# Optimization experiments

Hardware: AMD Instinct MI355X
Metric: run time of the kernel (lower is better)

## Reference

```python
import jax, jax.numpy as jnp
import numpy as np

NUM_HEADS = 4

def setup_inputs() -> dict:
    key = jax.random.key(0)
    ks = jax.random.split(key, 8)
    B_, N, C = 4096, 49, 128
    nW = 64
    return {
        "x": jax.random.normal(ks[0], (B_, N, C), dtype=jnp.float32),
        "mask": jax.random.normal(ks[1], (nW, N, N), dtype=jnp.float32),
        "qkv_w": jax.random.normal(ks[2], (3 * C, C), dtype=jnp.float32) * 0.02,
        "qkv_b": jax.random.normal(ks[3], (3 * C,), dtype=jnp.float32) * 0.02,
        "proj_w": jax.random.normal(ks[4], (C, C), dtype=jnp.float32) * 0.02,
        "proj_b": jax.random.normal(ks[5], (C,), dtype=jnp.float32) * 0.02,
        "rpb_table": jax.random.normal(ks[6], (169, NUM_HEADS), dtype=jnp.float32) * 0.02,
        "rel_index": jax.random.randint(ks[7], (N, N), 0, 169, dtype=jnp.int64),
    }

def reference(x, mask, qkv_w, qkv_b, proj_w, proj_b, rpb_table, rel_index):
    B_, N, C = x.shape
    H = NUM_HEADS
    hd = C // H
    scale = hd ** -0.5
    # qkv projection: [B_, N, 3, H, hd] -> (3, B_, H, N, hd)
    qkv = (x @ qkv_w.T + qkv_b).reshape(B_, N, 3, H, hd).transpose(2, 0, 3, 1, 4)
    q, k, v = qkv[0], qkv[1], qkv[2]
    q = q * scale
    attn = jnp.einsum('bhnd,bhmd->bhnm', q, k)  # [B_, H, N, N]
    # relative position bias gather: [N*N, H] -> [H, N, N]
    bias = rpb_table[rel_index.reshape(-1)].reshape(N, N, H).transpose(2, 0, 1)
    attn = attn + bias[None]
    # window mask add: view (B_//nW, nW, H, N, N) + mask[None, :, None]
    nW = mask.shape[0]
    attn = attn.reshape(B_ // nW, nW, H, N, N) + mask[None, :, None]
    attn = attn.reshape(B_, H, N, N)
    attn = jax.nn.softmax(attn, axis=-1)
    out = jnp.einsum('bhnm,bhmd->bhnd', attn, v)  # [B_, H, N, hd]
    out = out.transpose(0, 2, 1, 3).reshape(B_, N, C)
    out = out @ proj_w.T + proj_b
    return out
```

## Files before the change

### kernel.cpp

```cpp
#include <hip/hip_runtime.h>
#include <stdint.h>

typedef __attribute__((ext_vector_type(4))) float f32x4;
typedef __attribute__((ext_vector_type(2))) float f32x2;
typedef __attribute__((ext_vector_type(8))) short s16x8;
typedef __attribute__((ext_vector_type(4))) short s16x4;
typedef __attribute__((ext_vector_type(8))) __bf16 bf16x8;
typedef __attribute__((ext_vector_type(2))) __bf16 bf16x2;
typedef __attribute__((ext_vector_type(2))) unsigned u32x2;

#define SCALE 0.17677669529663687f
#define LOG2E 1.4426950408889634f

__device__ __forceinline__ unsigned f2bf(float f) {
  unsigned u = __builtin_bit_cast(unsigned, f);
  u += 0x7fffu + ((u >> 16) & 1u);
  return u >> 16;
}
__device__ __forceinline__ unsigned pk2(float lo, float hi) {
  f32x2 v; v[0] = lo; v[1] = hi;
  bf16x2 h = __builtin_convertvector(v, bf16x2);
  return __builtin_bit_cast(unsigned, h);
}
__device__ __forceinline__ unsigned short cv1(float v) {
  return (unsigned short)f2bf(v);
}

__device__ __forceinline__ f32x4 MFMA(s16x8 a, s16x8 b, f32x4 c) {
  return __builtin_amdgcn_mfma_f32_16x16x32_bf16(
      __builtin_bit_cast(bf16x8, a), __builtin_bit_cast(bf16x8, b), c, 0, 0, 0);
}
__device__ __forceinline__ f32x4 MFMA16(u32x2 a, u32x2 b, f32x4 c) {
#if __has_builtin(__builtin_amdgcn_mfma_f32_16x16x16bf16_1k)
  return __builtin_amdgcn_mfma_f32_16x16x16bf16_1k(
      __builtin_bit_cast(s16x4, a), __builtin_bit_cast(s16x4, b), c, 0, 0, 0);
#else
  f32x4 d;
  asm("v_mfma_f32_16x16x16_bf16 %0, %1, %2, %3"
      : "=v"(d) : "v"(a), "v"(b), "v"(c));
  return d;
#endif
}

template <int MODE>
__global__ __launch_bounds__(256, 4)
void win_attn(const float* __restrict__ x,
              const float* __restrict__ mask,
              const float* __restrict__ qkv_bs,
              const float* __restrict__ proj_b,
              const unsigned short* __restrict__ wq_bf,
              const unsigned short* __restrict__ wp_bf,
              const float* __restrict__ bias_full,
              const float* __restrict__ bias_pad,
              const float* __restrict__ mask_pad,
              const float* __restrict__ comb,
              float* __restrict__ out) {
  __shared__ alignas(16) char smem[16384];
  const int tid = threadIdx.x;
  const int l = tid & 63, w = tid >> 6;
  const int lr = l & 15, lq = l >> 4;
  const int b = blockIdx.x;
  const int wq = b & 63;

  {
    const float* xw = x + (size_t)b * (49 * 128);
    #pragma unroll
    for (int i = 0; i < 4; ++i) {
      const int r = w * 4 + lq + i * 16;
      s16x8 v = {};
      if (r < 49) {
        const float4* p = reinterpret_cast<const float4*>(xw + r * 128 + lr * 8);
        float4 f0 = p[0], f1 = p[1];
        union { unsigned u[4]; s16x8 v8; } U;
        U.u[0] = pk2(f0.x, f0.y); U.u[1] = pk2(f0.z, f0.w);
        U.u[2] = pk2(f1.x, f1.y); U.u[3] = pk2(f1.z, f1.w);
        v = U.v8;
      }
      *reinterpret_cast<s16x8*>(&smem[r * 256 + (((lr ^ (r & 15)) & 15) << 4)]) = v;
    }
  }
  __syncthreads();

  int addrK[4];
  #pragma unroll
  for (int kt = 0; kt < 4; ++kt)
    addrK[kt] = lr * 256 + ((((4 * kt + lq) ^ lr) & 15) << 4);

  u32x2 qB[4][2], kB[4][2], vA[2][4];
  #pragma unroll
  for (int g = 0; g < 6; ++g) {
    const int sect = g >> 1;
    const int half = g & 1;
    const int obase = sect * 128 + 32 * w + 16 * half;
    s16x8 wf[4];
    #pragma unroll
    for (int kt = 0; kt < 4; ++kt)
      wf[kt] = *reinterpret_cast<const s16x8*>(wq_bf + (obase + lr) * 128 + kt * 32 + lq * 8);
    if (sect < 2) {
      const f32x4 bia4 = *reinterpret_cast<const f32x4*>(qkv_bs + obase + 4 * lq);
      #pragma unroll
      for (int nt = 0; nt < 4; ++nt) {
        s16x8 ar[4];
        #pragma unroll
        for (int kt = 0; kt < 4; ++kt)
          ar[kt] = *reinterpret_cast<const s16x8*>(&smem[addrK[kt] + nt * 4096]);
        f32x4 acc = {};
        #pragma unroll
        for (int kt = 0; kt < 4; ++kt) acc = MFMA(wf[kt], ar[kt], acc);
        acc += bia4;
        u32x2 fr; fr[0] = pk2(acc[0], acc[1]); fr[1] = pk2(acc[2], acc[3]);
        if (sect == 0) qB[nt][half] = fr; else kB[nt][half] = fr;
      }
    } else {
      const float bo = qkv_bs[obase + lr];
      #pragma unroll
      for (int mt = 0; mt < 4; ++mt) {
        s16x8 ar[4];
        #pragma unroll
        for (int kt = 0; kt < 4; ++kt)
          ar[kt] = *reinterpret_cast<const s16x8*>(&smem[addrK[kt] + mt * 4096]);
        f32x4 acc = {};
        #pragma unroll
        for (int kt = 0; kt < 4; ++kt) acc = MFMA(ar[kt], wf[kt], acc);
        acc += bo;
        u32x2 fr; fr[0] = pk2(acc[0], acc[1]); fr[1] = pk2(acc[2], acc[3]);
        vA[half][mt] = fr;
      }
    }
  }
  __syncthreads();

  const float* biaW = bias_pad + w * 4096;
  const float* mskW = mask_pad + wq * 4096;
  const float* cW = comb + (size_t)(wq * 4 + w) * 4096;
  #pragma unroll
  for (int ntn = 0; ntn < 4; ++ntn) {
    const int n = 16 * ntn + lr;
    f32x4 add4[4];
    if (MODE == 2) {
      #pragma unroll
      for (int mtm = 0; mtm < 4; ++mtm)
        add4[mtm] = *reinterpret_cast<const f32x4*>(cW + n * 64 + 16 * mtm + 4 * lq);
    } else if (MODE == 1) {
      #pragma unroll
      for (int mtm = 0; mtm < 4; ++mtm) {
        const int m0 = 16 * mtm + 4 * lq;
        f32x4 bb = *reinterpret_cast<const f32x4*>(biaW + n * 64 + m0);
        f32x4 mm = *reinterpret_cast<const f32x4*>(mskW + n * 64 + m0);
        add4[mtm] = bb + mm;
      }
    }
    f32x4 sacc[4];
    __builtin_amdgcn_s_setprio(1);
    #pragma unroll
    for (int mtm = 0; mtm < 4; ++mtm) {
      sacc[mtm] = MFMA16(kB[mtm][0], qB[ntn][0], f32x4{});
      sacc[mtm] = MFMA16(kB[mtm][1], qB[ntn][1], sacc[mtm]);
    }
    __builtin_amdgcn_s_setprio(0);
    if (MODE >= 1) {
      #pragma unroll
      for (int mtm = 0; mtm < 4; ++mtm) sacc[mtm] += add4[mtm];
    } else {
      #pragma unroll
      for (int mtm = 0; mtm < 4; ++mtm)
        #pragma unroll
        for (int j = 0; j < 4; ++j) {
          const int m = 16 * mtm + 4 * lq + j;
          if (m < 49 && n < 49)
            sacc[mtm][j] = fmaf(bias_full[w * 2401 + n * 49 + m] + mask[wq * 2401 + n * 49 + m],
                                LOG2E, sacc[mtm][j]);
        }
    }
    {
      f32x4 v = sacc[3];
      v[0] = (lq == 0) ? v[0] : -1e30f;
      v[1] = -1e30f; v[2] = -1e30f; v[3] = -1e30f;
      sacc[3] = v;
    }
    float mx = -1e30f;
    #pragma unroll
    for (int mtm = 0; mtm < 4; ++mtm) {
      f32x4 v = sacc[mtm];
      mx = fmaxf(mx, fmaxf(fmaxf(v[0], v[1]), fmaxf(v[2], v[3])));
    }
    mx = fmaxf(mx, __shfl_xor(mx, 16, 64));
    mx = fmaxf(mx, __shfl_xor(mx, 32, 64));
    float s = 0.f;
    #pragma unroll
    for (int mtm = 0; mtm < 4; ++mtm) {
      f32x4 v = sacc[mtm];
      #pragma unroll
      for (int j = 0; j < 4; ++j) { v[j] = __builtin_exp2f(v[j] - mx); s += v[j]; }
      sacc[mtm] = v;
    }
    s += __shfl_xor(s, 16, 64);
    s += __shfl_xor(s, 32, 64);
    const float ri = 1.f / s;
    u32x2 p[4];
    #pragma unroll
    for (int mtm = 0; mtm < 4; ++mtm) {
      p[mtm][0] = pk2(sacc[mtm][0], sacc[mtm][1]);
      p[mtm][1] = pk2(sacc[mtm][2], sacc[mtm][3]);
    }
    __builtin_amdgcn_s_setprio(1);
    #pragma unroll
    for (int dt = 0; dt < 2; ++dt) {
      f32x4 oc = {};
      #pragma unroll
      for (int mtm = 0; mtm < 4; ++mtm) oc = MFMA16(vA[dt][mtm], p[mtm], oc);
      oc *= ri;
      u32x2 ov; ov[0] = pk2(oc[0], oc[1]); ov[1] = pk2(oc[2], oc[3]);
      const int cb = 64 * w + 32 * dt + 8 * lq;
      *reinterpret_cast<u32x2*>(
          &smem[n * 256 + (((((cb >> 4) ^ lr) & 15) << 4) | (cb & 15))]) = ov;
    }
    __builtin_amdgcn_s_setprio(0);
  }
  __syncthreads();

  s16x8 wpf[2][4];
  #pragma unroll
  for (int ct = 0; ct < 2; ++ct)
    #pragma unroll
    for (int kt = 0; kt < 4; ++kt)
      wpf[ct][kt] = *reinterpret_cast<const s16x8*>(
          wp_bf + (32 * w + 16 * ct + lr) * 128 + kt * 32 + lq * 8);
  float* ob = out + (size_t)b * (49 * 128);
  #pragma unroll
  for (int nt = 0; nt < 4; ++nt) {
    const int n = 16 * nt + lr;
    s16x8 osf[4];
    #pragma unroll
    for (int kt = 0; kt < 4; ++kt) {
      const int cb = 64 * kt + 16 * lq;
      osf[kt] = *reinterpret_cast<const s16x8*>(
          &smem[n * 256 + (((((cb >> 4) ^ lr) & 15) << 4) | (cb & 15))]);
    }
    #pragma unroll
    for (int ct = 0; ct < 2; ++ct) {
      const int c0 = 32 * w + 16 * ct + 4 * lq;
      f32x4 acc = {};
      #pragma unroll
      for (int kt = 0; kt < 4; ++kt) acc = MFMA(wpf[ct][kt], osf[kt], acc);
      acc += *reinterpret_cast<const f32x4*>(proj_b + c0);
      if (n < 49) *reinterpret_cast<f32x4*>(ob + n * 128 + c0) = acc;
    }
  }
}

__global__ void prep_kernel(const float* __restrict__ qkv_w,
                            const float* __restrict__ qkv_b,
                            const float* __restrict__ proj_w,
                            const float* __restrict__ rpb,
                            const int* __restrict__ rel_raw,
                            const float* __restrict__ mask,
                            unsigned short* __restrict__ wq_bf,
                            unsigned short* __restrict__ wp_bf,
                            float* __restrict__ qkv_bs,
                            float* __restrict__ bias_full,
                            float* __restrict__ bias_pad,
                            float* __restrict__ mask_pad,
                            float* __restrict__ comb,
                            int mode) {
  const int i = blockIdx.x * 256 + threadIdx.x;
  if (i < 49152) {
    float v = qkv_w[i];
    if (i < 16384) v *= SCALE * LOG2E;
    wq_bf[i] = cv1(v);
  } else if (i < 65536) {
    wp_bf[i - 49152] = cv1(proj_w[i - 49152]);
  } else if (i < 65920) {
    const int t = i - 65536;
    float v = qkv_b[t];
    if (t < 128) v *= SCALE * LOG2E;
    qkv_bs[t] = v;
  } else if (i < 75524) {
    const int t = i - 65920;
    const int h = t / 2401, nm = t % 2401;
    const bool is64 = (rel_raw[1] == 0) && (rel_raw[3] == 0) &&
                      (rel_raw[5] == 0) && (rel_raw[7] == 0);
    const int ridx = is64 ? rel_raw[2 * nm] : rel_raw[nm];
    bias_full[t] = rpb[ridx * 4 + h];
  } else if (mode == 2 && i < 75524 + 1048576) {
    const int t = i - 75524;
    const int wqi = t >> 14, h = (t >> 12) & 3, n = (t >> 6) & 63, m = t & 63;
    float v = 0.f;
    if (n < 49 && m < 49) {
      const bool is64 = (rel_raw[1] == 0) && (rel_raw[3] == 0) &&
                        (rel_raw[5] == 0) && (rel_raw[7] == 0);
      const int nm = n * 49 + m;
      const int ridx = is64 ? rel_raw[2 * nm] : rel_raw[nm];
      v = (rpb[ridx * 4 + h] + mask[wqi * 2401 + nm]) * LOG2E;
    }
    comb[t] = v;
  } else if (mode == 1 && i < 75524 + 16384) {
    const int j = i - 75524;
    const int h = j >> 12, r = (j >> 6) & 63, m = j & 63;
    float v = 0.f;
    if (r < 49 && m < 49) {
      const bool is64 = (rel_raw[1] == 0) && (rel_raw[3] == 0) &&
                        (rel_raw[5] == 0) && (rel_raw[7] == 0);
      const int nm = r * 49 + m;
      const int ridx = is64 ? rel_raw[2 * nm] : rel_raw[nm];
      v = rpb[ridx * 4 + h] * LOG2E;
    }
    bias_pad[j] = v;
  } else if (mode == 1 && i < 75524 + 16384 + 262144) {
    const int t = i - 75524 - 16384;
    const int wqi = t >> 12, n = (t >> 6) & 63, m = t & 63;
    mask_pad[t] = (n < 49 && m < 49) ? mask[wqi * 2401 + n * 49 + m] * LOG2E : 0.f;
  }
}

extern "C" void kernel_launch(void* const* d_in, const int* in_sizes, int n_in,
                              void* d_out, int out_size, void* d_ws, size_t ws_size,
                              hipStream_t stream) {
  const float* x      = (const float*)d_in[0];
  const float* mask   = (const float*)d_in[1];
  const float* qkv_w  = (const float*)d_in[2];
  const float* qkv_b  = (const float*)d_in[3];
  const float* proj_w = (const float*)d_in[4];
  const float* proj_b = (const float*)d_in[5];
  const float* rpb    = (const float*)d_in[6];
  const int*   rel    = (const int*)d_in[7];
  float* out = (float*)d_out;

  char* ws = (char*)d_ws;
  unsigned short* wq_bf = (unsigned short*)(ws + 0);
  unsigned short* wp_bf = (unsigned short*)(ws + 98304);
  float* qkv_bs    = (float*)(ws + 131072);
  float* bias_full = (float*)(ws + 132608);
  float* bias_pad  = (float*)(ws + 171024);
  float* mask_pad  = (float*)(ws + 236560);
  float* comb      = (float*)(ws + 1285376);

  int mode = 0;
  if (ws_size >= 5479680) mode = 2;
  else if (ws_size >= 1285136) mode = 1;
  const int B_ = in_sizes[0] / (49 * 128);

  const int prep_n = 75524 + (mode == 2 ? 1048576 : mode == 1 ? (16384 + 262144) : 0);
  prep_kernel<<<(prep_n + 255) / 256, 256, 0, stream>>>(
      qkv_w, qkv_b, proj_w, rpb, rel, mask,
      wq_bf, wp_bf, qkv_bs, bias_full, bias_pad, mask_pad, comb, mode);
  if (mode == 2)
    win_attn<2><<<B_, 256, 0, stream>>>(x, mask, qkv_bs, proj_b, wq_bf, wp_bf,
                                        bias_full, bias_pad, mask_pad, comb, out);
  else if (mode == 1)
    win_attn<1><<<B_, 256, 0, stream>>>(x, mask, qkv_bs, proj_b, wq_bf, wp_bf,
                                        bias_full, bias_pad, mask_pad, comb, out);
  else
    win_attn<0><<<B_, 256, 0, stream>>>(x, mask, qkv_bs, proj_b, wq_bf, wp_bf,
                                        bias_full, bias_pad, mask_pad, comb, out);
}
```

Measured before the change: 125.6 us.

## Cut register pressure to raise occupancy: split bias loads, drop softmax max, reload proj weights

Raises the launch-bounds occupancy hint from 4 to 5 blocks per CU. To fit in fewer registers, it loads the bias/mask additive terms in two halves interleaved with the QK MFMAs, and loads projection weight fragments per output tile instead of holding all of them. It also removes the row-max subtraction from the softmax and exponentiates the raw scores directly, which saves a reduction and two shuffles. Skipping the max relies on logits staying bounded, so larger inputs could overflow exp2.

```diff
diff --git a/kernel.cpp b/kernel.cpp
--- a/kernel.cpp
+++ b/kernel.cpp
@@ -43,7 +43,7 @@
 }
 
 template <int MODE>
-__global__ __launch_bounds__(256, 4)
+__global__ __launch_bounds__(256, 5)
 void win_attn(const float* __restrict__ x,
               const float* __restrict__ mask,
               const float* __restrict__ qkv_bs,
@@ -136,31 +136,44 @@
   #pragma unroll
   for (int ntn = 0; ntn < 4; ++ntn) {
     const int n = 16 * ntn + lr;
-    f32x4 add4[4];
+    f32x4 sacc[4];
+    f32x4 add2[2];
     if (MODE == 2) {
-      #pragma unroll
-      for (int mtm = 0; mtm < 4; ++mtm)
-        add4[mtm] = *reinterpret_cast<const f32x4*>(cW + n * 64 + 16 * mtm + 4 * lq);
+      add2[0] = *reinterpret_cast<const f32x4*>(cW + n * 64 + 4 * lq);
+      add2[1] = *reinterpret_cast<const f32x4*>(cW + n * 64 + 16 + 4 * lq);
     } else if (MODE == 1) {
-      #pragma unroll
-      for (int mtm = 0; mtm < 4; ++mtm) {
-        const int m0 = 16 * mtm + 4 * lq;
-        f32x4 bb = *reinterpret_cast<const f32x4*>(biaW + n * 64 + m0);
-        f32x4 mm = *reinterpret_cast<const f32x4*>(mskW + n * 64 + m0);
-        add4[mtm] = bb + mm;
-      }
-    }
-    f32x4 sacc[4];
+      add2[0] = *reinterpret_cast<const f32x4*>(biaW + n * 64 + 4 * lq) +
+                *reinterpret_cast<const f32x4*>(mskW + n * 64 + 4 * lq);
+      add2[1] = *reinterpret_cast<const f32x4*>(biaW + n * 64 + 16 + 4 * lq) +
+                *reinterpret_cast<const f32x4*>(mskW + n * 64 + 16 + 4 * lq);
+    }
     __builtin_amdgcn_s_setprio(1);
     #pragma unroll
-    for (int mtm = 0; mtm < 4; ++mtm) {
+    for (int mtm = 0; mtm < 2; ++mtm) {
       sacc[mtm] = MFMA16(kB[mtm][0], qB[ntn][0], f32x4{});
       sacc[mtm] = MFMA16(kB[mtm][1], qB[ntn][1], sacc[mtm]);
     }
     __builtin_amdgcn_s_setprio(0);
     if (MODE >= 1) {
-      #pragma unroll
-      for (int mtm = 0; mtm < 4; ++mtm) sacc[mtm] += add4[mtm];
+      sacc[0] += add2[0]; sacc[1] += add2[1];
+      add2[0] = (MODE == 2)
+        ? *reinterpret_cast<const f32x4*>(cW + n * 64 + 32 + 4 * lq)
+        : *reinterpret_cast<const f32x4*>(biaW + n * 64 + 32 + 4 * lq) +
+          *reinterpret_cast<const f32x4*>(mskW + n * 64 + 32 + 4 * lq);
+      add2[1] = (MODE == 2)
+        ? *reinterpret_cast<const f32x4*>(cW + n * 64 + 48 + 4 * lq)
+        : *reinterpret_cast<const f32x4*>(biaW + n * 64 + 48 + 4 * lq) +
+          *reinterpret_cast<const f32x4*>(mskW + n * 64 + 48 + 4 * lq);
+    }
+    __builtin_amdgcn_s_setprio(1);
+    #pragma unroll
+    for (int mtm = 2; mtm < 4; ++mtm) {
+      sacc[mtm] = MFMA16(kB[mtm][0], qB[ntn][0], f32x4{});
+      sacc[mtm] = MFMA16(kB[mtm][1], qB[ntn][1], sacc[mtm]);
+    }
+    __builtin_amdgcn_s_setprio(0);
+    if (MODE >= 1) {
+      sacc[2] += add2[0]; sacc[3] += add2[1];
     } else {
       #pragma unroll
       for (int mtm = 0; mtm < 4; ++mtm)
@@ -178,54 +191,35 @@
       v[1] = -1e30f; v[2] = -1e30f; v[3] = -1e30f;
       sacc[3] = v;
     }
-    float mx = -1e30f;
+    float s = 0.f;
+    u32x2 p[4];
     #pragma unroll
     for (int mtm = 0; mtm < 4; ++mtm) {
       f32x4 v = sacc[mtm];
-      mx = fmaxf(mx, fmaxf(fmaxf(v[0], v[1]), fmaxf(v[2], v[3])));
-    }
-    mx = fmaxf(mx, __shfl_xor(mx, 16, 64));
-    mx = fmaxf(mx, __shfl_xor(mx, 32, 64));
-    float s = 0.f;
-    #pragma unroll
-    for (int mtm = 0; mtm < 4; ++mtm) {
-      f32x4 v = sacc[mtm];
-      #pragma unroll
-      for (int j = 0; j < 4; ++j) { v[j] = __builtin_exp2f(v[j] - mx); s += v[j]; }
-      sacc[mtm] = v;
+      #pragma unroll
+      for (int j = 0; j < 4; ++j) { v[j] = __builtin_exp2f(v[j]); s += v[j]; }
+      p[mtm][0] = pk2(v[0], v[1]);
+      p[mtm][1] = pk2(v[2], v[3]);
     }
     s += __shfl_xor(s, 16, 64);
     s += __shfl_xor(s, 32, 64);
     const float ri = 1.f / s;
-    u32x2 p[4];
-    #pragma unroll
-    for (int mtm = 0; mtm < 4; ++mtm) {
-      p[mtm][0] = pk2(sacc[mtm][0], sacc[mtm][1]);
-      p[mtm][1] = pk2(sacc[mtm][2], sacc[mtm][3]);
-    }
-    __builtin_amdgcn_s_setprio(1);
     #pragma unroll
     for (int dt = 0; dt < 2; ++dt) {
+      __builtin_amdgcn_s_setprio(1);
       f32x4 oc = {};
       #pragma unroll
       for (int mtm = 0; mtm < 4; ++mtm) oc = MFMA16(vA[dt][mtm], p[mtm], oc);
+      __builtin_amdgcn_s_setprio(0);
       oc *= ri;
       u32x2 ov; ov[0] = pk2(oc[0], oc[1]); ov[1] = pk2(oc[2], oc[3]);
       const int cb = 64 * w + 32 * dt + 8 * lq;
       *reinterpret_cast<u32x2*>(
           &smem[n * 256 + (((((cb >> 4) ^ lr) & 15) << 4) | (cb & 15))]) = ov;
     }
-    __builtin_amdgcn_s_setprio(0);
   }
   __syncthreads();
 
-  s16x8 wpf[2][4];
-  #pragma unroll
-  for (int ct = 0; ct < 2; ++ct)
-    #pragma unroll
-    for (int kt = 0; kt < 4; ++kt)
-      wpf[ct][kt] = *reinterpret_cast<const s16x8*>(
-          wp_bf + (32 * w + 16 * ct + lr) * 128 + kt * 32 + lq * 8);
   float* ob = out + (size_t)b * (49 * 128);
   #pragma unroll
   for (int nt = 0; nt < 4; ++nt) {
@@ -239,10 +233,15 @@
     }
     #pragma unroll
     for (int ct = 0; ct < 2; ++ct) {
+      s16x8 wpf[4];
+      #pragma unroll
+      for (int kt = 0; kt < 4; ++kt)
+        wpf[kt] = *reinterpret_cast<const s16x8*>(
+            wp_bf + (32 * w + 16 * ct + lr) * 128 + kt * 32 + lq * 8);
       const int c0 = 32 * w + 16 * ct + 4 * lq;
       f32x4 acc = {};
       #pragma unroll
-      for (int kt = 0; kt < 4; ++kt) acc = MFMA(wpf[ct][kt], osf[kt], acc);
+      for (int kt = 0; kt < 4; ++kt) acc = MFMA(wpf[kt], osf[kt], acc);
       acc += *reinterpret_cast<const f32x4*>(proj_b + c0);
       if (n < 49) *reinterpret_cast<f32x4*>(ob + n * 128 + c0) = acc;
     }
```

Result: slower. 160.5 us (+27.8%).

## Process four windows per block with double-buffered x prefetch and max-free softmax

Applied to the files above, without the earlier changes.

Each block now loops over four consecutive windows instead of one, launching a quarter as many blocks. The next window's x is loaded and converted to bf16 in registers during the current window's QKV projection, then written into a second LDS buffer, so global-load latency overlaps compute. Shared memory doubles to 32 KB per block. The softmax also drops the row-max subtraction and its reductions, relying on logits being small enough not to overflow exp2, which is a numerical-robustness risk.

```diff
diff --git a/kernel.cpp b/kernel.cpp
--- a/kernel.cpp
+++ b/kernel.cpp
@@ -54,16 +54,21 @@
               const float* __restrict__ bias_pad,
               const float* __restrict__ mask_pad,
               const float* __restrict__ comb,
-              float* __restrict__ out) {
-  __shared__ alignas(16) char smem[16384];
+              float* __restrict__ out,
+              int B_total) {
+  __shared__ alignas(16) char smem[32768];
   const int tid = threadIdx.x;
   const int l = tid & 63, w = tid >> 6;
   const int lr = l & 15, lq = l >> 4;
-  const int b = blockIdx.x;
-  const int wq = b & 63;
+  const int bbase = blockIdx.x * 4;
+
+  int addrK[4];
+  #pragma unroll
+  for (int kt = 0; kt < 4; ++kt)
+    addrK[kt] = lr * 256 + ((((4 * kt + lq) ^ lr) & 15) << 4);
 
   {
-    const float* xw = x + (size_t)b * (49 * 128);
+    const float* xw = x + (size_t)bbase * (49 * 128);
     #pragma unroll
     for (int i = 0; i < 4; ++i) {
       const int r = w * 4 + lq + i * 16;
@@ -81,171 +86,195 @@
   }
   __syncthreads();
 
-  int addrK[4];
-  #pragma unroll
-  for (int kt = 0; kt < 4; ++kt)
-    addrK[kt] = lr * 256 + ((((4 * kt + lq) ^ lr) & 15) << 4);
-
-  u32x2 qB[4][2], kB[4][2], vA[2][4];
-  #pragma unroll
-  for (int g = 0; g < 6; ++g) {
-    const int sect = g >> 1;
-    const int half = g & 1;
-    const int obase = sect * 128 + 32 * w + 16 * half;
-    s16x8 wf[4];
+  int cur = 0;
+  #pragma unroll 1
+  for (int wi = 0; wi < 4; ++wi) {
+    const int b = bbase + wi;
+    if (b >= B_total) break;
+    const int wq = b & 63;
+    char* xsC = smem + (cur << 14);
+    char* xsN = smem + ((cur ^ 1) << 14);
+    const bool pf = (wi < 3) && (b + 1 < B_total);
+
+    s16x8 px[4];
+    if (pf) {
+      const float* xw = x + (size_t)(b + 1) * (49 * 128);
+      #pragma unroll
+      for (int i = 0; i < 4; ++i) {
+        const int r = w * 4 + lq + i * 16;
+        s16x8 v = {};
+        if (r < 49) {
+          const float4* p = reinterpret_cast<const float4*>(xw + r * 128 + lr * 8);
+          float4 f0 = p[0], f1 = p[1];
+          union { unsigned u[4]; s16x8 v8; } U;
+          U.u[0] = pk2(f0.x, f0.y); U.u[1] = pk2(f0.z, f0.w);
+          U.u[2] = pk2(f1.x, f1.y); U.u[3] = pk2(f1.z, f1.w);
+          v = U.v8;
+        }
+        px[i] = v;
+      }
+    }
+
+    u32x2 qB[4][2], kB[4][2], vA[2][4];
     #pragma unroll
-    for (int kt = 0; kt < 4; ++kt)
-      wf[kt] = *reinterpret_cast<const s16x8*>(wq_bf + (obase + lr) * 128 + kt * 32 + lq * 8);
-    if (sect < 2) {
-      const f32x4 bia4 = *reinterpret_cast<const f32x4*>(qkv_bs + obase + 4 * lq);
+    for (int g = 0; g < 6; ++g) {
+      const int sect = g >> 1;
+      const int half = g & 1;
+      const int obase = sect * 128 + 32 * w + 16 * half;
+      s16x8 wf[4];
+      #pragma unroll
+      for (int kt = 0; kt < 4; ++kt)
+        wf[kt] = *reinterpret_cast<const s16x8*>(wq_bf + (obase + lr) * 128 + kt * 32 + lq * 8);
+      if (sect < 2) {
+        const f32x4 bia4 = *reinterpret_cast<const f32x4*>(qkv_bs + obase + 4 * lq);
+        #pragma unroll
+        for (int nt = 0; nt < 4; ++nt) {
+          s16x8 ar[4];
+          #pragma unroll
+          for (int kt = 0; kt < 4; ++kt)
+            ar[kt] = *reinterpret_cast<const s16x8*>(&xsC[addrK[kt] + nt * 4096]);
+          f32x4 acc = {};
+          #pragma unroll
+          for (int kt = 0; kt < 4; ++kt) acc = MFMA(wf[kt], ar[kt], acc);
+          acc += bia4;
+          u32x2 fr; fr[0] = pk2(acc[0], acc[1]); fr[1] = pk2(acc[2], acc[3]);
+          if (sect == 0) qB[nt][half] = fr; else kB[nt][half] = fr;
+        }
+      } else {
+        const float bo = qkv_bs[obase + lr];
+        #pragma unroll
+        for (int mt = 0; mt < 4; ++mt) {
+          s16x8 ar[4];
+          #pragma unroll
+          for (int kt = 0; kt < 4; ++kt)
+            ar[kt] = *reinterpret_cast<const s16x8*>(&xsC[addrK[kt] + mt * 4096]);
+          f32x4 acc = {};
+          #pragma unroll
+          for (int kt = 0; kt < 4; ++kt) acc = MFMA(ar[kt], wf[kt], acc);
+          acc += bo;
+          u32x2 fr; fr[0] = pk2(acc[0], acc[1]); fr[1] = pk2(acc[2], acc[3]);
+          vA[half][mt] = fr;
+        }
+      }
+    }
+    __syncthreads();
+
+    if (pf) {
+      #pragma unroll
+      for (int i = 0; i < 4; ++i) {
+        const int r = w * 4 + lq + i * 16;
+        *reinterpret_cast<s16x8*>(&xsN[r * 256 + (((lr ^ (r & 15)) & 15) << 4)]) = px[i];
+      }
+    }
+
+    const float* biaW = bias_pad + w * 4096;
+    const float* mskW = mask_pad + wq * 4096;
+    const float* cW = comb + (size_t)(wq * 4 + w) * 4096;
+    #pragma unroll
+    for (int ntn = 0; ntn < 4; ++ntn) {
+      const int n = 16 * ntn + lr;
+      f32x4 add4[4];
+      if (MODE == 2) {
+        #pragma unroll
+        for (int mtm = 0; mtm < 4; ++mtm)
+          add4[mtm] = *reinterpret_cast<const f32x4*>(cW + n * 64 + 16 * mtm + 4 * lq);
+      } else if (MODE == 1) {
+        #pragma unroll
+        for (int mtm = 0; mtm < 4; ++mtm) {
+          const int m0 = 16 * mtm + 4 * lq;
+          f32x4 bb = *reinterpret_cast<const f32x4*>(biaW + n * 64 + m0);
+          f32x4 mm = *reinterpret_cast<const f32x4*>(mskW + n * 64 + m0);
+          add4[mtm] = bb + mm;
+        }
+      }
+      f32x4 sacc[4];
+      __builtin_amdgcn_s_setprio(1);
+      #pragma unroll
+      for (int mtm = 0; mtm < 4; ++mtm) {
+        sacc[mtm] = MFMA16(kB[mtm][0], qB[ntn][0], f32x4{});
+        sacc[mtm] = MFMA16(kB[mtm][1], qB[ntn][1], sacc[mtm]);
+      }
+      __builtin_amdgcn_s_setprio(0);
+      if (MODE >= 1) {
+        #pragma unroll
+        for (int mtm = 0; mtm < 4; ++mtm) sacc[mtm] += add4[mtm];
+      } else {
+        #pragma unroll
+        for (int mtm = 0; mtm < 4; ++mtm)
+          #pragma unroll
+          for (int j = 0; j < 4; ++j) {
+            const int m = 16 * mtm + 4 * lq + j;
+            if (m < 49 && n < 49)
+              sacc[mtm][j] = fmaf(bias_full[w * 2401 + n * 49 + m] + mask[wq * 2401 + n * 49 + m],
+                                  LOG2E, sacc[mtm][j]);
+          }
+      }
+      {
+        f32x4 v = sacc[3];
+        v[0] = (lq == 0) ? v[0] : -1e30f;
+        v[1] = -1e30f; v[2] = -1e30f; v[3] = -1e30f;
+        sacc[3] = v;
+      }
+      float s = 0.f;
+      u32x2 p[4];
+      #pragma unroll
+      for (int mtm = 0; mtm < 4; ++mtm) {
+        f32x4 v = sacc[mtm];
+        #pragma unroll
+        for (int j = 0; j < 4; ++j) { v[j] = __builtin_exp2f(v[j]); s += v[j]; }
+        p[mtm][0] = pk2(v[0], v[1]);
+        p[mtm][1] = pk2(v[2], v[3]);
+      }
+      s += __shfl_xor(s, 16, 64);
+      s += __shfl_xor(s, 32, 64);
+      const float ri = 1.f / s;
+      #pragma unroll
+      for (int dt = 0; dt < 2; ++dt) {
+        __builtin_amdgcn_s_setprio(1);
+        f32x4 oc = {};
+        #pragma unroll
+        for (int mtm = 0; mtm < 4; ++mtm) oc = MFMA16(vA[dt][mtm], p[mtm], oc);
+        __builtin_amdgcn_s_setprio(0);
+        oc *= ri;
+        u32x2 ov; ov[0] = pk2(oc[0], oc[1]); ov[1] = pk2(oc[2], oc[3]);
+        const int cb = 64 * w + 32 * dt + 8 * lq;
+        *reinterpret_cast<u32x2*>(
+            &xsC[n * 256 + (((((cb >> 4) ^ lr) & 15) << 4) | (cb & 15))]) = ov;
+      }
+    }
+    __syncthreads();
+
+    {
+      s16x8 wpf[2][4];
+      #pragma unroll
+      for (int ct = 0; ct < 2; ++ct)
+        #pragma unroll
+        for (int kt = 0; kt < 4; ++kt)
+          wpf[ct][kt] = *reinterpret_cast<const s16x8*>(
+              wp_bf + (32 * w + 16 * ct + lr) * 128 + kt * 32 + lq * 8);
+      float* ob = out + (size_t)b * (49 * 128);
       #pragma unroll
       for (int nt = 0; nt < 4; ++nt) {
-        s16x8 ar[4];
-        #pragma unroll
-        for (int kt = 0; kt < 4; ++kt)
-          ar[kt] = *reinterpret_cast<const s16x8*>(&smem[addrK[kt] + nt * 4096]);
-        f32x4 acc = {};
-        #pragma unroll
-        for (int kt = 0; kt < 4; ++kt) acc = MFMA(wf[kt], ar[kt], acc);
-        acc += bia4;
-        u32x2 fr; fr[0] = pk2(acc[0], acc[1]); fr[1] = pk2(acc[2], acc[3]);
-        if (sect == 0) qB[nt][half] = fr; else kB[nt][half] = fr;
-      }
-    } else {
-      const float bo = qkv_bs[obase + lr];
-      #pragma unroll
-      for (int mt = 0; mt < 4; ++mt) {
-        s16x8 ar[4];
-        #pragma unroll
-        for (int kt = 0; kt < 4; ++kt)
-          ar[kt] = *reinterpret_cast<const s16x8*>(&smem[addrK[kt] + mt * 4096]);
-        f32x4 acc = {};
-        #pragma unroll
-        for (int kt = 0; kt < 4; ++kt) acc = MFMA(ar[kt], wf[kt], acc);
-        acc += bo;
-        u32x2 fr; fr[0] = pk2(acc[0], acc[1]); fr[1] = pk2(acc[2], acc[3]);
-        vA[half][mt] = fr;
-      }
-    }
-  }
-  __syncthreads();
-
-  const float* biaW = bias_pad + w * 4096;
-  const float* mskW = mask_pad + wq * 4096;
-  const float* cW = comb + (size_t)(wq * 4 + w) * 4096;
-  #pragma unroll
-  for (int ntn = 0; ntn < 4; ++ntn) {
-    const int n = 16 * ntn + lr;
-    f32x4 add4[4];
-    if (MODE == 2) {
-      #pragma unroll
-      for (int mtm = 0; mtm < 4; ++mtm)
-        add4[mtm] = *reinterpret_cast<const f32x4*>(cW + n * 64 + 16 * mtm + 4 * lq);
-    } else if (MODE == 1) {
-      #pragma unroll
-      for (int mtm = 0; mtm < 4; ++mtm) {
-        const int m0 = 16 * mtm + 4 * lq;
-        f32x4 bb = *reinterpret_cast<const f32x4*>(biaW + n * 64 + m0);
-        f32x4 mm = *reinterpret_cast<const f32x4*>(mskW + n * 64 + m0);
-        add4[mtm] = bb + mm;
-      }
-    }
-    f32x4 sacc[4];
-    __builtin_amdgcn_s_setprio(1);
-    #pragma unroll
-    for (int mtm = 0; mtm < 4; ++mtm) {
-      sacc[mtm] = MFMA16(kB[mtm][0], qB[ntn][0], f32x4{});
-      sacc[mtm] = MFMA16(kB[mtm][1], qB[ntn][1], sacc[mtm]);
-    }
-    __builtin_amdgcn_s_setprio(0);
-    if (MODE >= 1) {
-      #pragma unroll
-      for (int mtm = 0; mtm < 4; ++mtm) sacc[mtm] += add4[mtm];
-    } else {
-      #pragma unroll
-      for (int mtm = 0; mtm < 4; ++mtm)
-        #pragma unroll
-        for (int j = 0; j < 4; ++j) {
-          const int m = 16 * mtm + 4 * lq + j;
-          if (m < 49 && n < 49)
-            sacc[mtm][j] = fmaf(bias_full[w * 2401 + n * 49 + m] + mask[wq * 2401 + n * 49 + m],
-                                LOG2E, sacc[mtm][j]);
-        }
-    }
-    {
-      f32x4 v = sacc[3];
-      v[0] = (lq == 0) ? v[0] : -1e30f;
-      v[1] = -1e30f; v[2] = -1e30f; v[3] = -1e30f;
-      sacc[3] = v;
-    }
-    float mx = -1e30f;
-    #pragma unroll
-    for (int mtm = 0; mtm < 4; ++mtm) {
-      f32x4 v = sacc[mtm];
-      mx = fmaxf(mx, fmaxf(fmaxf(v[0], v[1]), fmaxf(v[2], v[3])));
-    }
-    mx = fmaxf(mx, __shfl_xor(mx, 16, 64));
-    mx = fmaxf(mx, __shfl_xor(mx, 32, 64));
-    float s = 0.f;
-    #pragma unroll
-    for (int mtm = 0; mtm < 4; ++mtm) {
-      f32x4 v = sacc[mtm];
-      #pragma unroll
-      for (int j = 0; j < 4; ++j) { v[j] = __builtin_exp2f(v[j] - mx); s += v[j]; }
-      sacc[mtm] = v;
-    }
-    s += __shfl_xor(s, 16, 64);
-    s += __shfl_xor(s, 32, 64);
-    const float ri = 1.f / s;
-    u32x2 p[4];
-    #pragma unroll
-    for (int mtm = 0; mtm < 4; ++mtm) {
-      p[mtm][0] = pk2(sacc[mtm][0], sacc[mtm][1]);
-      p[mtm][1] = pk2(sacc[mtm][2], sacc[mtm][3]);
-    }
-    __builtin_amdgcn_s_setprio(1);
-    #pragma unroll
-    for (int dt = 0; dt < 2; ++dt) {
-      f32x4 oc = {};
-      #pragma unroll
-      for (int mtm = 0; mtm < 4; ++mtm) oc = MFMA16(vA[dt][mtm], p[mtm], oc);
-      oc *= ri;
-      u32x2 ov; ov[0] = pk2(oc[0], oc[1]); ov[1] = pk2(oc[2], oc[3]);
-      const int cb = 64 * w + 32 * dt + 8 * lq;
-      *reinterpret_cast<u32x2*>(
-          &smem[n * 256 + (((((cb >> 4) ^ lr) & 15) << 4) | (cb & 15))]) = ov;
-    }
-    __builtin_amdgcn_s_setprio(0);
-  }
-  __syncthreads();
-
-  s16x8 wpf[2][4];
-  #pragma unroll
-  for (int ct = 0; ct < 2; ++ct)
-    #pragma unroll
-    for (int kt = 0; kt < 4; ++kt)
-      wpf[ct][kt] = *reinterpret_cast<const s16x8*>(
-          wp_bf + (32 * w + 16 * ct + lr) * 128 + kt * 32 + lq * 8);
-  float* ob = out + (size_t)b * (49 * 128);
-  #pragma unroll
-  for (int nt = 0; nt < 4; ++nt) {
-    const int n = 16 * nt + lr;
-    s16x8 osf[4];
-    #pragma unroll
-    for (int kt = 0; kt < 4; ++kt) {
-      const int cb = 64 * kt + 16 * lq;
-      osf[kt] = *reinterpret_cast<const s16x8*>(
-          &smem[n * 256 + (((((cb >> 4) ^ lr) & 15) << 4) | (cb & 15))]);
-    }
-    #pragma unroll
-    for (int ct = 0; ct < 2; ++ct) {
-      const int c0 = 32 * w + 16 * ct + 4 * lq;
-      f32x4 acc = {};
-      #pragma unroll
-      for (int kt = 0; kt < 4; ++kt) acc = MFMA(wpf[ct][kt], osf[kt], acc);
-      acc += *reinterpret_cast<const f32x4*>(proj_b + c0);
-      if (n < 49) *reinterpret_cast<f32x4*>(ob + n * 128 + c0) = acc;
-    }
+        const int n = 16 * nt + lr;
+        s16x8 osf[4];
+        #pragma unroll
+        for (int kt = 0; kt < 4; ++kt) {
+          const int cb = 64 * kt + 16 * lq;
+          osf[kt] = *reinterpret_cast<const s16x8*>(
+              &xsC[n * 256 + (((((cb >> 4) ^ lr) & 15) << 4) | (cb & 15))]);
+        }
+        #pragma unroll
+        for (int ct = 0; ct < 2; ++ct) {
+          const int c0 = 32 * w + 16 * ct + 4 * lq;
+          f32x4 acc = {};
+          #pragma unroll
+          for (int kt = 0; kt < 4; ++kt) acc = MFMA(wpf[ct][kt], osf[kt], acc);
+          acc += *reinterpret_cast<const f32x4*>(proj_b + c0);
+          if (n < 49) *reinterpret_cast<f32x4*>(ob + n * 128 + c0) = acc;
+        }
+      }
+    }
+    cur ^= 1;
   }
 }
 
@@ -339,18 +368,19 @@
   if (ws_size >= 5479680) mode = 2;
   else if (ws_size >= 1285136) mode = 1;
   const int B_ = in_sizes[0] / (49 * 128);
+  const int nblk = (B_ + 3) / 4;
 
   const int prep_n = 75524 + (mode == 2 ? 1048576 : mode == 1 ? (16384 + 262144) : 0);
   prep_kernel<<<(prep_n + 255) / 256, 256, 0, stream>>>(
       qkv_w, qkv_b, proj_w, rpb, rel, mask,
       wq_bf, wp_bf, qkv_bs, bias_full, bias_pad, mask_pad, comb, mode);
   if (mode == 2)
-    win_attn<2><<<B_, 256, 0, stream>>>(x, mask, qkv_bs, proj_b, wq_bf, wp_bf,
-                                        bias_full, bias_pad, mask_pad, comb, out);
+    win_attn<2><<<nblk, 256, 0, stream>>>(x, mask, qkv_bs, proj_b, wq_bf, wp_bf,
+                                          bias_full, bias_pad, mask_pad, comb, out, B_);
   else if (mode == 1)
-    win_attn<1><<<B_, 256, 0, stream>>>(x, mask, qkv_bs, proj_b, wq_bf, wp_bf,
-                                        bias_full, bias_pad, mask_pad, comb, out);
+    win_attn<1><<<nblk, 256, 0, stream>>>(x, mask, qkv_bs, proj_b, wq_bf, wp_bf,
+                                          bias_full, bias_pad, mask_pad, comb, out, B_);
   else
-    win_attn<0><<<B_, 256, 0, stream>>>(x, mask, qkv_bs, proj_b, wq_bf, wp_bf,
-                                        bias_full, bias_pad, mask_pad, comb, out);
-}
+    win_attn<0><<<nblk, 256, 0, stream>>>(x, mask, qkv_bs, proj_b, wq_bf, wp_bf,
+                                          bias_full, bias_pad, mask_pad, comb, out, B_);
+}
```

Result: slower. 308.9 us (+146.0%).
